# Kernel tuning notes

Hardware: AMD Instinct MI355X
Metric: run time of the kernel (lower is better)

The kernel has to match this reference:

```python
import jax, jax.numpy as jnp
import numpy as np

N_NODES = 50000
N_EDGES = 800000
D_IN = 64
D_OUT = 64


def setup_inputs() -> dict:
    key = jax.random.key(0)
    ks = jax.random.split(key, 7)
    features = jax.random.normal(ks[0], (N_NODES, D_IN), dtype=jnp.float32)
    # Linear(in,out,bias=False) weight: (out_features, in_features)
    W = jax.random.normal(ks[1], (D_OUT, D_IN), dtype=jnp.float32) / np.sqrt(D_IN)
    bias = jnp.zeros((D_OUT,), dtype=jnp.float32)
    skip_weight = jnp.ones((D_OUT,), dtype=jnp.float32)
    # sparse normalized adjacency as an edge list with scalar weights
    edge_src = jax.random.randint(ks[2], (N_EDGES,), 0, N_NODES, dtype=jnp.int32)
    edge_dst = jax.random.randint(ks[3], (N_EDGES,), 0, N_NODES, dtype=jnp.int32)
    edge_weight = jax.random.uniform(ks[4], (N_EDGES,), dtype=jnp.float32)
    return {
        "features": features,
        "W": W,
        "bias": bias,
        "skip_weight": skip_weight,
        "edge_weight": edge_weight,
        "edge_src": edge_src,
        "edge_dst": edge_dst,
    }


def reference(features, W, bias, skip_weight, edge_weight, edge_src, edge_dst):
    # Feature transform: x @ W^T  -> (n, out_features)
    h = jnp.einsum("nd,od->no", features, W)
    # Skip term: elementwise scale of transformed features
    skip = h * skip_weight
    # Sparse SpMM: aggregate weighted neighbor messages
    msgs = h[edge_src] * edge_weight[:, None]          # (E, out)
    agg = jax.ops.segment_sum(msgs, edge_dst, num_segments=N_NODES)  # (n, out)
    out = skip + agg + bias
    return jax.nn.selu(out)
```

## Files before the change

### kernel.cpp

```cpp
#include <hip/hip_runtime.h>
#include <math.h>

#define N_NODES 50000
#define N_EDGES 800000
#define D 64
#define NB2 782
#define BCAP2 2048
#define EPB 4096
#define NSCAT 196
#define CAPB 32
#define SLAB (NSCAT * CAPB)
#define GROWS 128
#define GTILES 2
#define NGEMM 196

__device__ __forceinline__ float selu_f(float x) {
    const float scale = 1.0507009873554805f;
    const float alpha = 1.6732632423543772f;
    return x > 0.0f ? scale * x : scale * alpha * expm1f(x);
}

__device__ __forceinline__ unsigned int f2bf(float x) {
    unsigned int u = __float_as_uint(x);
    u += 0x7FFFu + ((u >> 16) & 1u);
    return u >> 16;
}

__device__ __forceinline__ float bf2f(unsigned int b) {
    return __uint_as_float(b << 16);
}

__global__ __launch_bounds__(1024) void fused_gemm_scatter(const float* __restrict__ feat,
                                                           const float* __restrict__ W,
                                                           const int* __restrict__ edst,
                                                           const int* __restrict__ esrc,
                                                           const float* __restrict__ ew,
                                                           unsigned short* __restrict__ hb,
                                                           int* __restrict__ cnts,
                                                           int2* __restrict__ pay) {
    extern __shared__ char smem[];
    const int tid = threadIdx.x;

    if (blockIdx.x < NSCAT) {
        int* hist    = (int*)smem;
        int* lexcl   = hist + NB2;
        int* waveAgg = lexcl + NB2;
        int2* stage  = (int2*)(waveAgg + 16);

        const int wid = tid >> 6;
        const int lane = tid & 63;
        const int e0 = blockIdx.x * EPB;
        const int cntb = min(EPB, N_EDGES - e0);

        for (int i = tid; i < NB2; i += 1024) hist[i] = 0;
        __syncthreads();

        int2 rec[4];
        int rb[4];
#pragma unroll
        for (int k = 0; k < 4; ++k) {
            const int idx = k * 1024 + tid;
            rb[k] = -1;
            if (idx < cntb) {
                const int e = e0 + idx;
                const int dst = edst[e];
                const int b = dst >> 6;
                rb[k] = b;
                rec[k] = make_int2((esrc[e] & 0xFFFF) | ((dst & 63) << 16) | (b << 22),
                                   __float_as_int(ew[e]));
                atomicAdd(&hist[b], 1);
            }
        }
        __syncthreads();

        const int v = (tid < NB2) ? hist[tid] : 0;
        int incl = v;
#pragma unroll
        for (int off = 1; off < 64; off <<= 1) {
            const int t = __shfl_up(incl, off);
            if (lane >= off) incl += t;
        }
        if (lane == 63) waveAgg[wid] = incl;
        __syncthreads();
        if (wid == 0) {
            const int wv = (lane < 16) ? waveAgg[lane] : 0;
            int wincl = wv;
#pragma unroll
            for (int off = 1; off < 16; off <<= 1) {
                const int t = __shfl_up(wincl, off);
                if (lane >= off) wincl += t;
            }
            if (lane < 16) waveAgg[lane] = wincl - wv;
        }
        __syncthreads();
        if (tid < NB2) {
            const int excl = incl - v + waveAgg[wid];
            lexcl[tid] = excl;
            hist[tid] = excl;
            cnts[blockIdx.x * NB2 + tid] = v;
        }
        __syncthreads();

#pragma unroll
        for (int k = 0; k < 4; ++k) {
            if (rb[k] >= 0) {
                const int p = atomicAdd(&hist[rb[k]], 1);
                stage[p] = rec[k];
            }
        }
        __syncthreads();

        for (int i = tid; i < cntb; i += 1024) {
            const int2 r = stage[i];
            const int b = ((unsigned int)r.x) >> 22;
            const int off = i - lexcl[b];
            if (off < CAPB) pay[(size_t)b * SLAB + blockIdx.x * CAPB + off] = r;
        }
    } else {
        float* Wt = (float*)smem;
        float* Sf = Wt + 64 * 68;
        const int gb = blockIdx.x - NSCAT;

        for (int i = tid; i < D * D; i += 1024) {
            int o = i >> 6, d = i & 63;
            Wt[d * 68 + o] = W[i];
        }

        const int r = tid >> 3;
        const int cg = tid & 7;

        for (int t = 0; t < GTILES; ++t) {
            const int base = gb * (GROWS * GTILES) + t * GROWS;
            if (base >= N_NODES) break;
            if (t) __syncthreads();

            for (int i = tid; i < GROWS * D; i += 1024) {
                int rr = i >> 6, cc = i & 63;
                int row = base + rr;
                Sf[rr * 68 + cc] = (row < N_NODES) ? feat[(size_t)row * D + cc] : 0.0f;
            }
            __syncthreads();

            const int row = base + r;
            if (row < N_NODES) {
                float4 a0 = {0, 0, 0, 0}, a1 = {0, 0, 0, 0};
                const float* WtC = Wt + cg * 8;
                const float* SfR = Sf + r * 68;
#pragma unroll 8
                for (int k = 0; k < D; ++k) {
                    const float f = SfR[k];
                    const float4 w0 = *(const float4*)(WtC + k * 68);
                    const float4 w1 = *(const float4*)(WtC + k * 68 + 4);
                    a0.x += f * w0.x; a0.y += f * w0.y; a0.z += f * w0.z; a0.w += f * w0.w;
                    a1.x += f * w1.x; a1.y += f * w1.y; a1.z += f * w1.z; a1.w += f * w1.w;
                }

                uint4 p;
                p.x = f2bf(a0.x) | (f2bf(a0.y) << 16);
                p.y = f2bf(a0.z) | (f2bf(a0.w) << 16);
                p.z = f2bf(a1.x) | (f2bf(a1.y) << 16);
                p.w = f2bf(a1.z) | (f2bf(a1.w) << 16);
                *(uint4*)(hb + (size_t)row * D + cg * 8) = p;
            }
        }
    }
}

__global__ __launch_bounds__(512) void sort_agg(const int* __restrict__ cnts,
                                                const int2* __restrict__ pay,
                                                const unsigned short* __restrict__ hb,
                                                const float* __restrict__ bias,
                                                const float* __restrict__ skipw,
                                                float* __restrict__ out) {
    __shared__ int2 stage[BCAP2];
    __shared__ int2 sorted[BCAP2];
    __shared__ int cntS[NSCAT];
    __shared__ int runoff[NSCAT];
    __shared__ int waveAgg[8];
    __shared__ int cntB[64], begB[64], curB[64];

    const int b = blockIdx.x;
    const int tid = threadIdx.x;
    const int wid = tid >> 6;
    const int lane = tid & 63;
    const int2* payb = pay + (size_t)b * SLAB;

    if (tid < 64) cntB[tid] = 0;

    const int c = (tid < NSCAT) ? cnts[tid * NB2 + b] : 0;

    int incl = c;
#pragma unroll
    for (int off = 1; off < 64; off <<= 1) {
        const int t = __shfl_up(incl, off);
        if (lane >= off) incl += t;
    }
    if (lane == 63) waveAgg[wid] = incl;
    __syncthreads();
    if (wid == 0) {
        const int wv = (lane < 8) ? waveAgg[lane] : 0;
        int wincl = wv;
#pragma unroll
        for (int off = 1; off < 8; off <<= 1) {
            const int t = __shfl_up(wincl, off);
            if (lane >= off) wincl += t;
        }
        if (lane < 8) waveAgg[lane] = wincl - wv;
    }
    __syncthreads();
    if (tid < NSCAT) {
        cntS[tid] = c;
        runoff[tid] = incl - c + waveAgg[wid];
    }
    __syncthreads();

    for (int i = tid; i < NSCAT * CAPB; i += 512) {
        const int blk = i >> 5;
        const int pos = i & (CAPB - 1);
        if (pos < cntS[blk]) {
            const int p = runoff[blk] + pos;
            if (p < BCAP2) {
                const int2 r = payb[i];
                stage[p] = r;
                atomicAdd(&cntB[(r.x >> 16) & 63], 1);
            }
        }
    }
    __syncthreads();

    const int total = min(runoff[NSCAT - 1] + cntS[NSCAT - 1], BCAP2);

    if (tid < 64) {
        const int v = cntB[tid];
        int inc2 = v;
#pragma unroll
        for (int off = 1; off < 64; off <<= 1) {
            const int t = __shfl_up(inc2, off);
            if (tid >= off) inc2 += t;
        }
        const int excl = inc2 - v;
        begB[tid] = excl;
        curB[tid] = excl;
    }
    __syncthreads();

    for (int i = tid; i < total; i += 512) {
        const int2 r = stage[i];
        const int p = atomicAdd(&curB[(r.x >> 16) & 63], 1);
        sorted[p] = r;
    }
    __syncthreads();

    const int half = lane >> 5;
    const int sl = lane & 31;
    const float2 kv = ((const float2*)skipw)[sl];
    const float2 bv = ((const float2*)bias)[sl];

    for (int nn = 0; nn < 8; ++nn) {
        const int nl = wid * 8 + nn;
        const int node = (b << 6) + nl;
        if (node >= N_NODES) break;

        const int beg = begB[nl];
        const int deg = cntB[nl];

        float a0x = 0.f, a0y = 0.f, a1x = 0.f, a1y = 0.f;
        float a2x = 0.f, a2y = 0.f, a3x = 0.f, a3y = 0.f;

        int j = 0;
        for (; j + 7 < deg; j += 8) {
            const int2 r0 = sorted[beg + j + 0 + half];
            const int2 r1 = sorted[beg + j + 2 + half];
            const int2 r2 = sorted[beg + j + 4 + half];
            const int2 r3 = sorted[beg + j + 6 + half];
            const unsigned int g0 = *(const unsigned int*)(hb + ((size_t)(r0.x & 0xFFFF) << 6) + sl * 2);
            const unsigned int g1 = *(const unsigned int*)(hb + ((size_t)(r1.x & 0xFFFF) << 6) + sl * 2);
            const unsigned int g2 = *(const unsigned int*)(hb + ((size_t)(r2.x & 0xFFFF) << 6) + sl * 2);
            const unsigned int g3 = *(const unsigned int*)(hb + ((size_t)(r3.x & 0xFFFF) << 6) + sl * 2);
            const float w0 = __int_as_float(r0.y);
            const float w1 = __int_as_float(r1.y);
            const float w2 = __int_as_float(r2.y);
            const float w3 = __int_as_float(r3.y);
            a0x += bf2f(g0 & 0xFFFF) * w0;  a0y += bf2f(g0 >> 16) * w0;
            a1x += bf2f(g1 & 0xFFFF) * w1;  a1y += bf2f(g1 >> 16) * w1;
            a2x += bf2f(g2 & 0xFFFF) * w2;  a2y += bf2f(g2 >> 16) * w2;
            a3x += bf2f(g3 & 0xFFFF) * w3;  a3y += bf2f(g3 >> 16) * w3;
        }
        for (; j + 1 < deg; j += 2) {
            const int2 r = sorted[beg + j + half];
            const unsigned int g = *(const unsigned int*)(hb + ((size_t)(r.x & 0xFFFF) << 6) + sl * 2);
            const float w = __int_as_float(r.y);
            a0x += bf2f(g & 0xFFFF) * w;  a0y += bf2f(g >> 16) * w;
        }
        if (j < deg) {
            const int2 r = sorted[beg + j];
            const unsigned int g = *(const unsigned int*)(hb + ((size_t)(r.x & 0xFFFF) << 6) + sl * 2);
            const float w = __int_as_float(r.y);
            const float m = (half == 0) ? 1.0f : 0.0f;
            a1x += bf2f(g & 0xFFFF) * w * m;  a1y += bf2f(g >> 16) * w * m;
        }

        float sx = (a0x + a1x) + (a2x + a3x);
        float sy = (a0y + a1y) + (a2y + a3y);
        sx += __shfl_xor(sx, 32);
        sy += __shfl_xor(sy, 32);

        if (half == 0) {
            const unsigned int hn = *(const unsigned int*)(hb + ((size_t)node << 6) + sl * 2);
            float2 o;
            o.x = selu_f(bf2f(hn & 0xFFFF) * kv.x + bv.x + sx);
            o.y = selu_f(bf2f(hn >> 16) * kv.y + bv.y + sy);
            ((float2*)(out + ((size_t)node << 6)))[sl] = o;
        }
    }
}

extern "C" void kernel_launch(void* const* d_in, const int* in_sizes, int n_in,
                              void* d_out, int out_size, void* d_ws, size_t ws_size,
                              hipStream_t stream) {
    const float* feat  = (const float*)d_in[0];
    const float* W     = (const float*)d_in[1];
    const float* bias  = (const float*)d_in[2];
    const float* skipw = (const float*)d_in[3];
    const float* ew    = (const float*)d_in[4];
    const int*   esrc  = (const int*)d_in[5];
    const int*   edst  = (const int*)d_in[6];
    float* out = (float*)d_out;

    int2*           pay  = (int2*)d_ws;
    unsigned short* hb   = (unsigned short*)(pay + (size_t)NB2 * SLAB);
    int*            cnts = (int*)(hb + (size_t)N_NODES * D);

    const size_t smem = (size_t)(64 * 68 + GROWS * 68) * sizeof(float);
    fused_gemm_scatter<<<NSCAT + NGEMM, 1024, smem, stream>>>(feat, W, edst, esrc, ew,
                                                              hb, cnts, pay);

    sort_agg<<<NB2, 512, 0, stream>>>(cnts, pay, hb, bias, skipw, out);
}
```

Baseline: 124.9 us.

## Register-block GEMM as 4x4 outer products and drop staging buffer in sort_agg

The GEMM blocks now process 256 rows at once, with K split into two halves. Features are stored transposed in shared memory so each thread computes a 4x4 output tile from float4 loads of both operands, which raises FLOPs per LDS load. sort_agg drops the intermediate stage buffer and reads the payload from global memory twice (count pass, then scatter pass), which halves its shared memory and may raise occupancy. The cost is extra global reads of the payload and a changed overflow check: entries are now dropped by sorted position rather than by staged position.

```diff
diff --git a/kernel.cpp b/kernel.cpp
--- a/kernel.cpp
+++ b/kernel.cpp
@@ -10,9 +10,10 @@
 #define NSCAT 196
 #define CAPB 32
 #define SLAB (NSCAT * CAPB)
-#define GROWS 128
-#define GTILES 2
+#define GR2 256
 #define NGEMM 196
+#define SFT_LD 264
+#define WTO_LD 68
 
 __device__ __forceinline__ float selu_f(float x) {
     const float scale = 1.0507009873554805f;
@@ -117,51 +118,65 @@
             if (off < CAPB) pay[(size_t)b * SLAB + blockIdx.x * CAPB + off] = r;
         }
     } else {
-        float* Wt = (float*)smem;
-        float* Sf = Wt + 64 * 68;
-        const int gb = blockIdx.x - NSCAT;
+        float* Sft = (float*)smem;
+        float* Wto = Sft + 32 * SFT_LD;
+        const int base = (blockIdx.x - NSCAT) * GR2;
 
         for (int i = tid; i < D * D; i += 1024) {
-            int o = i >> 6, d = i & 63;
-            Wt[d * 68 + o] = W[i];
-        }
-
-        const int r = tid >> 3;
-        const int cg = tid & 7;
-
-        for (int t = 0; t < GTILES; ++t) {
-            const int base = gb * (GROWS * GTILES) + t * GROWS;
-            if (base >= N_NODES) break;
-            if (t) __syncthreads();
-
-            for (int i = tid; i < GROWS * D; i += 1024) {
-                int rr = i >> 6, cc = i & 63;
-                int row = base + rr;
-                Sf[rr * 68 + cc] = (row < N_NODES) ? feat[(size_t)row * D + cc] : 0.0f;
+            const int o = i >> 6, k = i & 63;
+            Wto[k * WTO_LD + o] = W[i];
+        }
+
+        const int rg = tid >> 4;
+        const int cg = tid & 15;
+
+        float a0x=0,a0y=0,a0z=0,a0w=0, a1x=0,a1y=0,a1z=0,a1w=0;
+        float a2x=0,a2y=0,a2z=0,a2w=0, a3x=0,a3y=0,a3z=0,a3w=0;
+
+        for (int kh = 0; kh < 2; ++kh) {
+            if (kh) __syncthreads();
+
+            for (int t = tid; t < GR2 * 8; t += 1024) {
+                const int row = t >> 3, kq = t & 7;
+                const int grow = base + row;
+                float4 v = make_float4(0.f, 0.f, 0.f, 0.f);
+                if (grow < N_NODES)
+                    v = *(const float4*)(feat + (size_t)grow * D + kh * 32 + kq * 4);
+                Sft[(kq * 4 + 0) * SFT_LD + row] = v.x;
+                Sft[(kq * 4 + 1) * SFT_LD + row] = v.y;
+                Sft[(kq * 4 + 2) * SFT_LD + row] = v.z;
+                Sft[(kq * 4 + 3) * SFT_LD + row] = v.w;
             }
             __syncthreads();
 
-            const int row = base + r;
-            if (row < N_NODES) {
-                float4 a0 = {0, 0, 0, 0}, a1 = {0, 0, 0, 0};
-                const float* WtC = Wt + cg * 8;
-                const float* SfR = Sf + r * 68;
 #pragma unroll 8
-                for (int k = 0; k < D; ++k) {
-                    const float f = SfR[k];
-                    const float4 w0 = *(const float4*)(WtC + k * 68);
-                    const float4 w1 = *(const float4*)(WtC + k * 68 + 4);
-                    a0.x += f * w0.x; a0.y += f * w0.y; a0.z += f * w0.z; a0.w += f * w0.w;
-                    a1.x += f * w1.x; a1.y += f * w1.y; a1.z += f * w1.z; a1.w += f * w1.w;
-                }
-
-                uint4 p;
-                p.x = f2bf(a0.x) | (f2bf(a0.y) << 16);
-                p.y = f2bf(a0.z) | (f2bf(a0.w) << 16);
-                p.z = f2bf(a1.x) | (f2bf(a1.y) << 16);
-                p.w = f2bf(a1.z) | (f2bf(a1.w) << 16);
-                *(uint4*)(hb + (size_t)row * D + cg * 8) = p;
-            }
+            for (int k = 0; k < 32; ++k) {
+                const float4 av = *(const float4*)(Sft + k * SFT_LD + rg * 4);
+                const float4 bv = *(const float4*)(Wto + (kh * 32 + k) * WTO_LD + cg * 4);
+                a0x += av.x * bv.x; a0y += av.x * bv.y; a0z += av.x * bv.z; a0w += av.x * bv.w;
+                a1x += av.y * bv.x; a1y += av.y * bv.y; a1z += av.y * bv.z; a1w += av.y * bv.w;
+                a2x += av.z * bv.x; a2y += av.z * bv.y; a2z += av.z * bv.z; a2w += av.z * bv.w;
+                a3x += av.w * bv.x; a3y += av.w * bv.y; a3z += av.w * bv.z; a3w += av.w * bv.w;
+            }
+        }
+
+        const int r0 = base + rg * 4;
+        uint2 p;
+        if (r0 + 0 < N_NODES) {
+            p.x = f2bf(a0x) | (f2bf(a0y) << 16); p.y = f2bf(a0z) | (f2bf(a0w) << 16);
+            *(uint2*)(hb + (size_t)(r0 + 0) * D + cg * 4) = p;
+        }
+        if (r0 + 1 < N_NODES) {
+            p.x = f2bf(a1x) | (f2bf(a1y) << 16); p.y = f2bf(a1z) | (f2bf(a1w) << 16);
+            *(uint2*)(hb + (size_t)(r0 + 1) * D + cg * 4) = p;
+        }
+        if (r0 + 2 < N_NODES) {
+            p.x = f2bf(a2x) | (f2bf(a2y) << 16); p.y = f2bf(a2z) | (f2bf(a2w) << 16);
+            *(uint2*)(hb + (size_t)(r0 + 2) * D + cg * 4) = p;
+        }
+        if (r0 + 3 < N_NODES) {
+            p.x = f2bf(a3x) | (f2bf(a3y) << 16); p.y = f2bf(a3z) | (f2bf(a3w) << 16);
+            *(uint2*)(hb + (size_t)(r0 + 3) * D + cg * 4) = p;
         }
     }
 }
@@ -172,7 +187,6 @@
                                                 const float* __restrict__ bias,
                                                 const float* __restrict__ skipw,
                                                 float* __restrict__ out) {
-    __shared__ int2 stage[BCAP2];
     __shared__ int2 sorted[BCAP2];
     __shared__ int cntS[NSCAT];
     __shared__ int runoff[NSCAT];
@@ -218,17 +232,11 @@
         const int blk = i >> 5;
         const int pos = i & (CAPB - 1);
         if (pos < cntS[blk]) {
-            const int p = runoff[blk] + pos;
-            if (p < BCAP2) {
-                const int2 r = payb[i];
-                stage[p] = r;
-                atomicAdd(&cntB[(r.x >> 16) & 63], 1);
-            }
-        }
-    }
-    __syncthreads();
-
-    const int total = min(runoff[NSCAT - 1] + cntS[NSCAT - 1], BCAP2);
+            const int2 r = payb[i];
+            atomicAdd(&cntB[(r.x >> 16) & 63], 1);
+        }
+    }
+    __syncthreads();
 
     if (tid < 64) {
         const int v = cntB[tid];
@@ -244,10 +252,14 @@
     }
     __syncthreads();
 
-    for (int i = tid; i < total; i += 512) {
-        const int2 r = stage[i];
-        const int p = atomicAdd(&curB[(r.x >> 16) & 63], 1);
-        sorted[p] = r;
+    for (int i = tid; i < NSCAT * CAPB; i += 512) {
+        const int blk = i >> 5;
+        const int pos = i & (CAPB - 1);
+        if (pos < cntS[blk]) {
+            const int2 r = payb[i];
+            const int p = atomicAdd(&curB[(r.x >> 16) & 63], 1);
+            if (p < BCAP2) sorted[p] = r;
+        }
     }
     __syncthreads();
 
@@ -331,7 +343,7 @@
     unsigned short* hb   = (unsigned short*)(pay + (size_t)NB2 * SLAB);
     int*            cnts = (int*)(hb + (size_t)N_NODES * D);
 
-    const size_t smem = (size_t)(64 * 68 + GROWS * 68) * sizeof(float);
+    const size_t smem = (size_t)(32 * SFT_LD + 64 * WTO_LD) * sizeof(float);
     fused_gemm_scatter<<<NSCAT + NGEMM, 1024, smem, stream>>>(feat, W, edst, esrc, ew,
                                                               hb, cnts, pay);
 
```

New measurement: 122.7 us. About the same (-1.7%).
